# Kernel tuning notes

Measured on AMD Instinct MI355X. Metric: run time of the kernel, lower is better.

Reference implementation:

```python
import jax, jax.numpy as jnp
import numpy as np

H = 64

def _gru(x, Wih, Whh, bih, bhh):
    # x: [NB, L, D]; torch GRU gate order: r, z, n
    h0 = jnp.zeros((x.shape[0], Whh.shape[1]), x.dtype)
    def step(h, xt):
        gi = xt @ Wih.T + bih
        gh = h @ Whh.T + bhh
        ir, iz, inn = jnp.split(gi, 3, axis=-1)
        hr, hz, hn = jnp.split(gh, 3, axis=-1)
        r = jax.nn.sigmoid(ir + hr)
        z = jax.nn.sigmoid(iz + hz)
        n = jnp.tanh(inn + r * hn)
        h_new = (1.0 - z) * n + z * h
        return h_new, h_new
    hT, ys = jax.lax.scan(step, h0, jnp.swapaxes(x, 0, 1))
    return jnp.swapaxes(ys, 0, 1), hT  # outputs [NB,L,H], last hidden [NB,H]


def setup_inputs() -> dict:
    key = jax.random.key(0)
    ks = jax.random.split(key, 20)
    N, B, L, D = 2000, 8, 12, 2
    E = 16000
    s = 0.1
    return {
        "data": jax.random.normal(ks[0], (N, B, L, D), jnp.float32),
        "features": jax.random.normal(ks[1], (N, H), jnp.float32),
        "edge_index": jax.random.randint(ks[2], (2, E), 0, N, jnp.int64 if jax.config.jax_enable_x64 else jnp.int32),
        "Wih1": jax.random.normal(ks[3], (3 * H, D), jnp.float32) * s,
        "Whh1": jax.random.normal(ks[4], (3 * H, H), jnp.float32) * s,
        "bih1": jax.random.normal(ks[5], (3 * H,), jnp.float32) * s,
        "bhh1": jax.random.normal(ks[6], (3 * H,), jnp.float32) * s,
        "W1": jax.random.normal(ks[7], (16, 2 * H), jnp.float32) * s,
        "b1": jax.random.normal(ks[8], (16,), jnp.float32) * s,
        "W2": jax.random.normal(ks[9], (2, 16), jnp.float32) * s,
        "b2": jax.random.normal(ks[10], (2,), jnp.float32) * s,
        "W3": jax.random.normal(ks[11], (2 * H * H, 2), jnp.float32) * s,
        "b3": jax.random.normal(ks[12], (2 * H * H,), jnp.float32) * s,
        "Wih2": jax.random.normal(ks[13], (3 * H, H), jnp.float32) * s,
        "Whh2": jax.random.normal(ks[14], (3 * H, H), jnp.float32) * s,
        "bih2": jax.random.normal(ks[15], (3 * H,), jnp.float32) * s,
        "bhh2": jax.random.normal(ks[16], (3 * H,), jnp.float32) * s,
    }


def reference(data, features, edge_index, Wih1, Whh1, bih1, bhh1,
              W1, b1, W2, b2, W3, b3, Wih2, Whh2, bih2, bhh2):
    N, B, L, D = data.shape
    # --- first GRU over [N*B, L, D] ---
    out1, h1 = _gru(data.reshape(N * B, L, D), Wih1, Whh1, bih1, bhh1)
    out1 = out1.reshape(N, B, L, H)
    h1 = h1.reshape(N, B, H)
    # --- MetaGAT with self loops ---
    loops = jnp.arange(N, dtype=edge_index.dtype)
    src = jnp.concatenate([edge_index[0], loops])  # j (source)
    dst = jnp.concatenate([edge_index[1], loops])  # i (target)
    states_j = out1[src]                 # [E', B, L, H]
    states_i = out1[dst]
    feats = jnp.concatenate([features[dst], features[src]], axis=-1)  # [E', 2H]
    # per-edge MLP generating weights
    hdn = jax.nn.sigmoid(feats @ W1.T + b1)
    hdn = jax.nn.sigmoid(hdn @ W2.T + b2)
    w = (hdn @ W3.T + b3).reshape(-1, 2 * H, H)  # [E', 2H, H]
    states = jnp.concatenate([states_i, states_j], axis=-1)  # [E', B, L, 2H]
    alpha = jax.nn.leaky_relu(jnp.einsum('eblk,ekh->eblh', states, w))
    alpha = jax.nn.softmax(alpha, axis=1)  # softmax over batch dim, as in source
    msg = alpha * states_j                 # [E', B, L, H]
    agg = jax.ops.segment_sum(msg, dst, num_segments=N)
    out2 = jax.nn.relu(agg)                # [N, B, L, H]
    # --- second GRU ---
    _, h2 = _gru(out2.reshape(N * B, L, H), Wih2, Whh2, bih2, bhh2)
    h2 = h2.reshape(N, B, H)
    return h1, h2
```

## Files before the change

kernel.cpp:

```cpp
#include <hip/hip_runtime.h>
#include <hip/hip_bf16.h>

typedef unsigned short ushort_t;
typedef unsigned int uint_t;
typedef __attribute__((ext_vector_type(8))) short bf16x8;
typedef __attribute__((ext_vector_type(4))) float f32x4;

#define NNODE 2000
#define NB 8
#define LSEQ 12
#define HDIM 64
#define NEDGE 16000
#define NSEQ (NNODE * NB)
#define OUT1_ELEMS (NNODE * NB * LSEQ * HDIM)
#define OUT1_BYTES (OUT1_ELEMS * 2)
#define AGG_BYTES  (OUT1_ELEMS * 2)
#define SST 72
#define LOG2E 1.4426950408889634f

#define WFRAG_ELEMS (6 * 2 * 256 * 8)
#define G2FRAG_ELEMS (3 * 2 * 2 * 256 * 8)

__device__ __forceinline__ float bf1(ushort_t u) { return __uint_as_float(((uint_t)u) << 16); }
__device__ __forceinline__ ushort_t fbf(float f) {
    uint_t x = __float_as_uint(f);
    uint_t r = x + 0x7fffu + ((x >> 16) & 1u);
    return (ushort_t)(r >> 16);
}
__device__ __forceinline__ float sigm(float x) {
    return __builtin_amdgcn_rcpf(1.f + __expf(-x));
}
__device__ __forceinline__ float tanh_fast(float x) {
    return 2.f * __builtin_amdgcn_rcpf(1.f + __expf(-2.f * x)) - 1.f;
}


__global__ __launch_bounds__(256) void mega_kernel(
    const float* __restrict__ data, const float* __restrict__ Wih,
    const float* __restrict__ Whh, const float* __restrict__ bih,
    const float* __restrict__ bhh, ushort_t* __restrict__ out1,
    float* __restrict__ h1out,
    const int* __restrict__ edges, int* __restrict__ degree,
    int* __restrict__ rowstart, int* __restrict__ srcids,
    int* __restrict__ eids, int* __restrict__ order,
    const float* __restrict__ features,
    const float* __restrict__ W1, const float* __restrict__ b1,
    const float* __restrict__ W2, const float* __restrict__ b2,
    float* __restrict__ alphas,
    const float* __restrict__ W3, const float* __restrict__ b3,
    const float* __restrict__ Wih2, const float* __restrict__ Whh2,
    ushort_t* __restrict__ wfrag, ushort_t* __restrict__ g2frag)
{
    __shared__ ushort_t H[2][16][SST] __attribute__((aligned(16)));
    __shared__ float XD[16][26];
    __shared__ int hist[NNODE];
    __shared__ int wsum[4];
    __shared__ float m1[4][16];
    __shared__ int dh[64];

    const int bx = blockIdx.x;
    const int tid = threadIdx.x;

    if (bx == 5501) {
        {
            const int wv = tid >> 6, r = tid & 15, quad = (tid >> 4) & 3;
            const int n = wv * 16 + r;
#pragma unroll
            for (int ks = 0; ks < 2; ++ks) {
                ushort_t ta[8], tb[8], tc[8], ba[8], bb[8], bc[8];
#pragma unroll
                for (int jj = 0; jj < 8; ++jj) {
                    const int mt_ = (ks * 32 + quad * 8 + jj) * 64 + n;
                    float2 w2 = ((const float2*)W3)[mt_];
                    ta[jj] = fbf(w2.x * LOG2E); tb[jj] = fbf(w2.y * LOG2E);
                    tc[jj] = fbf(b3[mt_] * LOG2E);
                    const int mb_ = (64 + ks * 32 + quad * 8 + jj) * 64 + n;
                    float2 w2b = ((const float2*)W3)[mb_];
                    ba[jj] = fbf(w2b.x * LOG2E); bb[jj] = fbf(w2b.y * LOG2E);
                    bc[jj] = fbf(b3[mb_] * LOG2E);
                }
                *(uint4*)(wfrag + ((0 * 2 + ks) * 256 + tid) * 8) = *(uint4*)ta;
                *(uint4*)(wfrag + ((1 * 2 + ks) * 256 + tid) * 8) = *(uint4*)tb;
                *(uint4*)(wfrag + ((2 * 2 + ks) * 256 + tid) * 8) = *(uint4*)tc;
                *(uint4*)(wfrag + ((3 * 2 + ks) * 256 + tid) * 8) = *(uint4*)ba;
                *(uint4*)(wfrag + ((4 * 2 + ks) * 256 + tid) * 8) = *(uint4*)bb;
                *(uint4*)(wfrag + ((5 * 2 + ks) * 256 + tid) * 8) = *(uint4*)bc;
            }
        }
        {
            const int nw = tid >> 6, c = tid & 15, quad = (tid >> 4) & 3;
            const int j = nw * 16 + c;
#pragma unroll
            for (int g = 0; g < 3; ++g) {
                const int row = g * 64 + j;
#pragma unroll
                for (int ks = 0; ks < 2; ++ks) {
                    const float* wp = Whh2 + (row << 6) + ks * 32 + quad * 8;
                    float4 wa = *(const float4*)wp;
                    float4 wb = *(const float4*)(wp + 4);
                    ushort_t tmp[8];
                    tmp[0] = fbf(wa.x); tmp[1] = fbf(wa.y); tmp[2] = fbf(wa.z); tmp[3] = fbf(wa.w);
                    tmp[4] = fbf(wb.x); tmp[5] = fbf(wb.y); tmp[6] = fbf(wb.z); tmp[7] = fbf(wb.w);
                    *(uint4*)(g2frag + (((g * 2 + ks) * 2 + 0) * 256 + tid) * 8) = *(uint4*)tmp;
                    const float* wp2 = Wih2 + (row << 6) + ks * 32 + quad * 8;
                    float4 va = *(const float4*)wp2;
                    float4 vb = *(const float4*)(wp2 + 4);
                    tmp[0] = fbf(va.x); tmp[1] = fbf(va.y); tmp[2] = fbf(va.z); tmp[3] = fbf(va.w);
                    tmp[4] = fbf(vb.x); tmp[5] = fbf(vb.y); tmp[6] = fbf(vb.z); tmp[7] = fbf(vb.w);
                    *(uint4*)(g2frag + (((g * 2 + ks) * 2 + 1) * 256 + tid) * 8) = *(uint4*)tmp;
                }
            }
        }
        return;
    }

    if (bx == 1000) {
        for (int k = tid; k < NNODE; k += 256) hist[k] = 0;
        if (tid < 64) dh[tid] = 0;
        __syncthreads();
        for (int it = 0; it < 16; ++it) {
            const int e0 = it * 1024 + tid * 4;
            if (e0 + 3 < NEDGE) {
                int4 v4 = *(const int4*)(edges + NEDGE + e0);
                atomicAdd(&hist[v4.x], 1);
                atomicAdd(&hist[v4.y], 1);
                atomicAdd(&hist[v4.z], 1);
                atomicAdd(&hist[v4.w], 1);
            } else {
#pragma unroll
                for (int k = 0; k < 4; ++k) {
                    const int e = e0 + k;
                    if (e < NEDGE) atomicAdd(&hist[edges[NEDGE + e]], 1);
                }
            }
        }
        __syncthreads();
        const int lane = tid & 63, w = tid >> 6;
        int d[8];
        int s = 0;
#pragma unroll
        for (int q = 0; q < 8; ++q) {
            const int idx = tid * 8 + q;
            d[q] = (idx < NNODE) ? hist[idx] : 0;
            s += d[q];
        }
        int v = s;
#pragma unroll
        for (int off = 1; off < 64; off <<= 1) {
            int u = __shfl_up(v, off);
            if (lane >= off) v += u;
        }
        if (lane == 63) wsum[w] = v;
        __syncthreads();
        int base = 0;
        for (int k = 0; k < 4; ++k) if (k < w) base += wsum[k];
        int run = base + v - s;
        int rs8[8];
#pragma unroll
        for (int q = 0; q < 8; ++q) {
            const int idx = tid * 8 + q;
            if (idx < NNODE) {
                rs8[q] = run;
                rowstart[idx] = run;
                degree[idx] = d[q];
                run += d[q];
                atomicAdd(&dh[63 - min(d[q], 63)], 1);
            }
        }
        __syncthreads();
        if (tid == 0) {
            int acc = 0;
            for (int k = 0; k < 64; ++k) { const int c = dh[k]; dh[k] = acc; acc += c; }
        }
        __syncthreads();
#pragma unroll
        for (int q = 0; q < 8; ++q) {
            const int idx = tid * 8 + q;
            if (idx < NNODE) {
                const int pos = atomicAdd(&dh[63 - min(d[q], 63)], 1);
                order[pos] = idx;
            }
        }
        __syncthreads();
#pragma unroll
        for (int q = 0; q < 8; ++q) {
            const int idx = tid * 8 + q;
            if (idx < NNODE) hist[idx] = rs8[q];
        }
        __syncthreads();
        for (int it = 0; it < 16; ++it) {
            const int e0 = it * 1024 + tid * 4;
            if (e0 + 3 < NEDGE) {
                int4 dv4 = *(const int4*)(edges + NEDGE + e0);
                int4 sv4 = *(const int4*)(edges + e0);
                int pos;
                pos = atomicAdd(&hist[dv4.x], 1); srcids[pos] = sv4.x; eids[pos] = e0;
                pos = atomicAdd(&hist[dv4.y], 1); srcids[pos] = sv4.y; eids[pos] = e0 + 1;
                pos = atomicAdd(&hist[dv4.z], 1); srcids[pos] = sv4.z; eids[pos] = e0 + 2;
                pos = atomicAdd(&hist[dv4.w], 1); srcids[pos] = sv4.w; eids[pos] = e0 + 3;
            } else {
#pragma unroll
                for (int k = 0; k < 4; ++k) {
                    const int e = e0 + k;
                    if (e < NEDGE) {
                        const int pos = atomicAdd(&hist[edges[NEDGE + e]], 1);
                        srcids[pos] = edges[e];
                        eids[pos] = e;
                    }
                }
            }
        }
        return;
    }

    if (bx > 1000) {
        const int w = tid >> 6, lane = tid & 63;
        const int e = (bx - 1001) * 4 + w;
        int i, j;
        if (e < NEDGE) { j = edges[e]; i = edges[NEDGE + e]; }
        else { i = j = e - NEDGE; }
        const int o = lane >> 2, q = lane & 3;
        const float* fsrc = (q < 2) ? (features + i * 64 + q * 32)
                                    : (features + j * 64 + (q - 2) * 32);
        const float* wsrc = W1 + o * 128 + q * 32;
        float acc = 0.f;
#pragma unroll
        for (int k = 0; k < 32; ++k) acc += fsrc[k] * wsrc[k];
        acc += __shfl_xor(acc, 1);
        acc += __shfl_xor(acc, 2);
        if (q == 0) m1[w][o] = sigm(acc + b1[o]);
        __syncthreads();
        if (lane < 32 && e < NEDGE + NNODE) {
            const int o2 = lane >> 4, k = lane & 15;
            float p = m1[w][k] * W2[o2 * 16 + k];
            p += __shfl_xor(p, 1);
            p += __shfl_xor(p, 2);
            p += __shfl_xor(p, 4);
            p += __shfl_xor(p, 8);
            if (k == 0) alphas[e * 2 + o2] = sigm(p + b2[o2]);
        }
        return;
    }

    const int nw = tid >> 6;
    const int c = tid & 15;
    const int quad = (tid >> 4) & 3;
    const int j = nw * 16 + c;
    const int s0 = bx * 16;
    const int crow = tid >> 4, ccol = (tid & 15) * 4;

    if (tid < 128) *(uint4*)&H[0][tid >> 3][(tid & 7) * 8] = uint4{0, 0, 0, 0};
#pragma unroll
    for (int p = 0; p < 2; ++p) {
        const int flat = p * 256 + tid;
        if (flat < 384) {
            const int sl = flat / 24, q = flat - sl * 24;
            XD[sl][q] = data[(s0 + sl) * 24 + q];
        }
    }

    bf16x8 Bh[3][2];
    float wi0[3], wi1[3], bi[3], bh[3];
#pragma unroll
    for (int g = 0; g < 3; ++g) {
        const int row = g * 64 + j;
        float2 wi = *(const float2*)(Wih + row * 2);
        wi0[g] = wi.x; wi1[g] = wi.y;
        bi[g] = bih[row]; bh[g] = bhh[row];
#pragma unroll
        for (int ks = 0; ks < 2; ++ks) {
            const float* wp = Whh + (row << 6) + ks * 32 + quad * 8;
            float4 wa = *(const float4*)wp;
            float4 wb = *(const float4*)(wp + 4);
            ushort_t tmp[8];
            tmp[0] = fbf(wa.x); tmp[1] = fbf(wa.y); tmp[2] = fbf(wa.z); tmp[3] = fbf(wa.w);
            tmp[4] = fbf(wb.x); tmp[5] = fbf(wb.y); tmp[6] = fbf(wb.z); tmp[7] = fbf(wb.w);
            Bh[g][ks] = *(bf16x8*)tmp;
        }
    }

    float hold[4];
#pragma unroll
    for (int rg = 0; rg < 4; ++rg) hold[rg] = 0.f;

    for (int t = 0; t < LSEQ; ++t) {
        __syncthreads();
        const ushort_t (*Hr)[SST] = H[t & 1];
        ushort_t (*Hw)[SST] = H[1 - (t & 1)];
        bf16x8 a0 = *(const bf16x8*)&Hr[c][quad * 8];
        bf16x8 a1 = *(const bf16x8*)&Hr[c][32 + quad * 8];
        if (t > 0)
            *(uint2*)(out1 + (s0 + crow) * (LSEQ * HDIM) + (t - 1) * HDIM + ccol) =
                *(const uint2*)&Hr[crow][ccol];
        f32x4 gh[3];
#pragma unroll
        for (int g = 0; g < 3; ++g) {
            f32x4 acc = {0.f, 0.f, 0.f, 0.f};
            acc = __builtin_amdgcn_mfma_f32_16x16x32_bf16(a0, Bh[g][0], acc, 0, 0, 0);
            acc = __builtin_amdgcn_mfma_f32_16x16x32_bf16(a1, Bh[g][1], acc, 0, 0, 0);
            gh[g] = acc;
        }
#pragma unroll
        for (int rg = 0; rg < 4; ++rg) {
            const int sloc = quad * 4 + rg;
            float2 xp = *(const float2*)&XD[sloc][2 * t];
            float gr = bh[0] + gh[0][rg];
            float gz = bh[1] + gh[1][rg];
            float gn = bh[2] + gh[2][rg];
            float ir = bi[0] + wi0[0] * xp.x + wi1[0] * xp.y;
            float iz = bi[1] + wi0[1] * xp.x + wi1[1] * xp.y;
            float in = bi[2] + wi0[2] * xp.x + wi1[2] * xp.y;
            float r = sigm(ir + gr);
            float z = sigm(iz + gz);
            float n = tanh_fast(in + r * gn);
            float hv = (1.f - z) * n + z * hold[rg];
            hold[rg] = hv;
            Hw[sloc][j] = fbf(hv);
        }
    }
    __syncthreads();
    *(uint2*)(out1 + (s0 + crow) * (LSEQ * HDIM) + (LSEQ - 1) * HDIM + ccol) =
        *(const uint2*)&H[LSEQ & 1][crow][ccol];
#pragma unroll
    for (int rg = 0; rg < 4; ++rg) {
        const int sloc = quad * 4 + rg;
        h1out[(s0 + sloc) * HDIM + j] = hold[rg];
    }
}

__global__ __launch_bounds__(256) void gat_csr_kernel(
    const ushort_t* __restrict__ out1,
    const int* __restrict__ degree, const int* __restrict__ rowstart,
    const int* __restrict__ srcids, const int* __restrict__ eids,
    const int* __restrict__ order,
    const float* __restrict__ alphas,
    const ushort_t* __restrict__ wfrag,
    ushort_t* __restrict__ agg)
{
    __shared__ ushort_t POOL[4][32][SST] __attribute__((aligned(16)));

    const int tid = threadIdx.x;
    const int i = order[blockIdx.x];
    const int mh = blockIdx.y;
    const int deg = degree[i];
    const int rs = rowstart[i];

    const int wv = tid >> 6;
    const int r = tid & 15;
    const int quad = (tid >> 4) & 3;
    const int n = wv * 16 + r;

    const float2 aSelf = *(const float2*)(alphas + (NEDGE + i) * 2);

    int glo[2], lso[2];
#pragma unroll
    for (int p = 0; p < 2; ++p) {
        const int u = p * 256 + tid;
        const int rr = u >> 4, c4 = u & 15;
        const int b = rr & 7, l = (rr >> 3) + 4 * mh;
        glo[p] = (b * 12 + l) * 64 + c4 * 4;
        lso[p] = rr * SST + c4 * 4;
    }
    int afo[2][2];
#pragma unroll
    for (int mt = 0; mt < 2; ++mt) {
        afo[mt][0] = (mt * 16 + r) * SST + quad * 8;
        afo[mt][1] = afo[mt][0] + 32;
    }
    int cbo[2];
#pragma unroll
    for (int mt = 0; mt < 2; ++mt)
        cbo[mt] = (mt * 16 + quad * 4) * SST + (n & ~1);
    const uint_t shamt = (n & 1) ? 0u : 16u;

    const ushort_t* pi = out1 + i * (NB * LSEQ * HDIM);
    ushort_t* const sbase = &POOL[0][0][0];
    ushort_t* const Si = sbase;

#pragma unroll
    for (int p = 0; p < 2; ++p)
        *(uint2*)(Si + lso[p]) = *(const uint2*)(pi + glo[p]);

    bf16x8 WtA[2], WtB[2], WtC[2], WbA[2], WbB[2], WbC[2];
#pragma unroll
    for (int ks = 0; ks < 2; ++ks) {
        WtA[ks] = *(const bf16x8*)(wfrag + ((0 * 2 + ks) * 256 + tid) * 8);
        WtB[ks] = *(const bf16x8*)(wfrag + ((1 * 2 + ks) * 256 + tid) * 8);
        WtC[ks] = *(const bf16x8*)(wfrag + ((2 * 2 + ks) * 256 + tid) * 8);
        WbA[ks] = *(const bf16x8*)(wfrag + ((3 * 2 + ks) * 256 + tid) * 8);
        WbB[ks] = *(const bf16x8*)(wfrag + ((4 * 2 + ks) * 256 + tid) * 8);
        WbC[ks] = *(const bf16x8*)(wfrag + ((5 * 2 + ks) * 256 + tid) * 8);
    }

    __syncthreads();

    f32x4 PA[2], PB[2], PC[2];
#pragma unroll
    for (int mt = 0; mt < 2; ++mt) {
        bf16x8 af0 = *(const bf16x8*)(Si + afo[mt][0]);
        bf16x8 af1 = *(const bf16x8*)(Si + afo[mt][1]);
        f32x4 pa = {0.f, 0.f, 0.f, 0.f};
        f32x4 pb = {0.f, 0.f, 0.f, 0.f};
        f32x4 pc = {0.f, 0.f, 0.f, 0.f};
        pa = __builtin_amdgcn_mfma_f32_16x16x32_bf16(af0, WtA[0], pa, 0, 0, 0);
        pa = __builtin_amdgcn_mfma_f32_16x16x32_bf16(af1, WtA[1], pa, 0, 0, 0);
        pb = __builtin_amdgcn_mfma_f32_16x16x32_bf16(af0, WtB[0], pb, 0, 0, 0);
        pb = __builtin_amdgcn_mfma_f32_16x16x32_bf16(af1, WtB[1], pb, 0, 0, 0);
        pc = __builtin_amdgcn_mfma_f32_16x16x32_bf16(af0, WtC[0], pc, 0, 0, 0);
        pc = __builtin_amdgcn_mfma_f32_16x16x32_bf16(af1, WtC[1], pc, 0, 0, 0);
        PA[mt] = pa; PB[mt] = pb; PC[mt] = pc;
    }

    float accN[2][4];
#pragma unroll
    for (int mt = 0; mt < 2; ++mt)
#pragma unroll
        for (int g2 = 0; g2 < 4; ++g2) accN[mt][g2] = 0.f;

    auto process = [&](const ushort_t* SB, float2 a01) {
#pragma unroll
        for (int mt = 0; mt < 2; ++mt) {
            bf16x8 aj0 = *(const bf16x8*)(SB + afo[mt][0]);
            bf16x8 aj1 = *(const bf16x8*)(SB + afo[mt][1]);
            const uint_t* dp = (const uint_t*)(SB + cbo[mt]);
            uint_t d0 = dp[0], d1 = dp[36], d2 = dp[72], d3 = dp[108];
            f32x4 aA = PA[mt], aB = PB[mt], aC = PC[mt];
            aA = __builtin_amdgcn_mfma_f32_16x16x32_bf16(aj0, WbA[0], aA, 0, 0, 0);
            aA = __builtin_amdgcn_mfma_f32_16x16x32_bf16(aj1, WbA[1], aA, 0, 0, 0);
            aB = __builtin_amdgcn_mfma_f32_16x16x32_bf16(aj0, WbB[0], aB, 0, 0, 0);
            aB = __builtin_amdgcn_mfma_f32_16x16x32_bf16(aj1, WbB[1], aB, 0, 0, 0);
            aC = __builtin_amdgcn_mfma_f32_16x16x32_bf16(aj0, WbC[0], aC, 0, 0, 0);
            aC = __builtin_amdgcn_mfma_f32_16x16x32_bf16(aj1, WbC[1], aC, 0, 0, 0);
            float v[4];
            float s = 0.f;
#pragma unroll
            for (int g2 = 0; g2 < 4; ++g2) {
                float x = fmaf(a01.x, aA[g2], fmaf(a01.y, aB[g2], aC[g2]));
                x = fmaxf(x, 0.01f * x);
                v[g2] = __builtin_amdgcn_exp2f(x);
                s += v[g2];
            }
            s += __shfl_xor(s, 16);
            const float inv = __builtin_amdgcn_rcpf(s);
            uint_t dd[4] = {d0, d1, d2, d3};
#pragma unroll
            for (int g2 = 0; g2 < 4; ++g2) {
                const float sj = __uint_as_float((dd[g2] << shamt) & 0xFFFF0000u);
                accN[mt][g2] += v[g2] * inv * sj;
            }
        }
    };

    int sa_nxt = 0, sb_nxt = 0, eA1 = 0, eB1 = 0;
    float2 aA_cur = float2{0.f, 0.f}, aB_cur = float2{0.f, 0.f};
    if (deg >= 1) { const int e = eids[rs];     aA_cur = *(const float2*)(alphas + e * 2); }
    if (deg >= 2) { const int e = eids[rs + 1]; aB_cur = *(const float2*)(alphas + e * 2); }
    if (deg >= 3) { sa_nxt = srcids[rs + 2]; eA1 = eids[rs + 2]; }
    if (deg >= 4) { sb_nxt = srcids[rs + 3]; eB1 = eids[rs + 3]; }

    uint2 pfA[2], pfB[2];
    {
        const ushort_t* pA = out1 + ((deg >= 1) ? srcids[rs] : 0) * (NB * LSEQ * HDIM);
        const ushort_t* pB = out1 + ((deg >= 2) ? srcids[rs + 1] : 0) * (NB * LSEQ * HDIM);
#pragma unroll
        for (int p = 0; p < 2; ++p) {
            pfA[p] = *(const uint2*)(pA + glo[p]);
            pfB[p] = *(const uint2*)(pB + glo[p]);
        }
    }

    process(Si, aSelf);
    __syncthreads();

    const int npairs = (deg + 1) >> 1;
    for (int pk = 0; pk < npairs; ++pk) {
        ushort_t* SA = sbase + (2 * (pk & 1)) * (32 * SST);
        ushort_t* SB = SA + 32 * SST;
#pragma unroll
        for (int p = 0; p < 2; ++p) {
            *(uint2*)(SA + lso[p]) = pfA[p];
            *(uint2*)(SB + lso[p]) = pfB[p];
        }
        const int base = pk * 2;
        const bool hasB = (base + 1) < deg;

        int sa_n2 = 0, sb_n2 = 0, eA2 = 0, eB2 = 0;
        if (base + 4 < deg) { sa_n2 = srcids[rs + base + 4]; eA2 = eids[rs + base + 4]; }
        if (base + 5 < deg) { sb_n2 = srcids[rs + base + 5]; eB2 = eids[rs + base + 5]; }
        float2 aA_n = float2{0.f, 0.f}, aB_n = float2{0.f, 0.f};
        if (base + 2 < deg) aA_n = *(const float2*)(alphas + eA1 * 2);
        if (base + 3 < deg) aB_n = *(const float2*)(alphas + eB1 * 2);

        __syncthreads();

        if (base + 2 < deg) {
            const ushort_t* pA = out1 + sa_nxt * (NB * LSEQ * HDIM);
#pragma unroll
            for (int p = 0; p < 2; ++p) pfA[p] = *(const uint2*)(pA + glo[p]);
        }
        if (base + 3 < deg) {
            const ushort_t* pB = out1 + sb_nxt * (NB * LSEQ * HDIM);
#pragma unroll
            for (int p = 0; p < 2; ++p) pfB[p] = *(const uint2*)(pB + glo[p]);
        }

        process(SA, aA_cur);
        if (hasB) process(SB, aB_cur);

        aA_cur = aA_n; aB_cur = aB_n;
        sa_nxt = sa_n2; sb_nxt = sb_n2;
        eA1 = eA2; eB1 = eB2;
    }

#pragma unroll
    for (int mt = 0; mt < 2; ++mt)
#pragma unroll
        for (int g2 = 0; g2 < 4; ++g2) {
            const int gr = mh * 32 + mt * 16 + quad * 4 + g2;
            const int b = gr & 7, l = gr >> 3;
            agg[(i * 96 + b * 12 + l) * 64 + n] = fbf(accN[mt][g2]);
        }
}

__global__ __launch_bounds__(256) void gru2_kernel(
    const ushort_t* __restrict__ agg, const ushort_t* __restrict__ g2frag,
    const float* __restrict__ bih, const float* __restrict__ bhh,
    float* __restrict__ h2out)
{
    __shared__ ushort_t H[2][16][SST] __attribute__((aligned(16)));
    __shared__ ushort_t X[2][16][SST] __attribute__((aligned(16)));

    const int tid = threadIdx.x;
    const int nw = tid >> 6;
    const int c = tid & 15;
    const int quad = (tid >> 4) & 3;
    const int j = nw * 16 + c;
    const int s0 = blockIdx.x * 16;
    const int sl = tid >> 3, k0 = (tid & 7) * 8;

    if (tid < 128) *(uint4*)&H[0][tid >> 3][(tid & 7) * 8] = uint4{0, 0, 0, 0};

    bf16x8 Bh[3][2], Bi[3][2];
    float bi[3], bh[3];
#pragma unroll
    for (int g = 0; g < 3; ++g) {
        const int row = g * 64 + j;
        bi[g] = bih[row]; bh[g] = bhh[row];
#pragma unroll
        for (int ks = 0; ks < 2; ++ks) {
            Bh[g][ks] = *(const bf16x8*)(g2frag + (((g * 2 + ks) * 2 + 0) * 256 + tid) * 8);
            Bi[g][ks] = *(const bf16x8*)(g2frag + (((g * 2 + ks) * 2 + 1) * 256 + tid) * 8);
        }
    }

    float hold[4];
#pragma unroll
    for (int rg = 0; rg < 4; ++rg) hold[rg] = 0.f;

    if (tid < 128) {
        ushort_t xr[8];
        *(uint4*)xr = *(const uint4*)(agg + (s0 + sl) * (LSEQ * HDIM) + k0);
        ushort_t xs[8];
#pragma unroll
        for (int q = 0; q < 8; ++q) xs[q] = (xr[q] & 0x8000u) ? (ushort_t)0 : xr[q];
        *(uint4*)&X[0][sl][k0] = *(uint4*)xs;
    }

    for (int t = 0; t < LSEQ; ++t) {
        __syncthreads();
        const int rb = t & 1, wb = 1 - rb;
        bf16x8 ah0 = *(const bf16x8*)&H[rb][c][quad * 8];
        bf16x8 ah1 = *(const bf16x8*)&H[rb][c][32 + quad * 8];
        bf16x8 ax0 = *(const bf16x8*)&X[rb][c][quad * 8];
        bf16x8 ax1 = *(const bf16x8*)&X[rb][c][32 + quad * 8];

        ushort_t xr[8];
        if (t < LSEQ - 1 && tid < 128)
            *(uint4*)xr = *(const uint4*)(agg + (s0 + sl) * (LSEQ * HDIM) +
                                          (t + 1) * HDIM + k0);

        f32x4 gh[3], gi[3];
#pragma unroll
        for (int g = 0; g < 3; ++g) {
            f32x4 acc = {0.f, 0.f, 0.f, 0.f};
            acc = __builtin_amdgcn_mfma_f32_16x16x32_bf16(ah0, Bh[g][0], acc, 0, 0, 0);
            acc = __builtin_amdgcn_mfma_f32_16x16x32_bf16(ah1, Bh[g][1], acc, 0, 0, 0);
            gh[g] = acc;
            f32x4 acc2 = {0.f, 0.f, 0.f, 0.f};
            acc2 = __builtin_amdgcn_mfma_f32_16x16x32_bf16(ax0, Bi[g][0], acc2, 0, 0, 0);
            acc2 = __builtin_amdgcn_mfma_f32_16x16x32_bf16(ax1, Bi[g][1], acc2, 0, 0, 0);
            gi[g] = acc2;
        }
#pragma unroll
        for (int rg = 0; rg < 4; ++rg) {
            const int sloc = quad * 4 + rg;
            float r = sigm(bi[0] + gi[0][rg] + bh[0] + gh[0][rg]);
            float z = sigm(bi[1] + gi[1][rg] + bh[1] + gh[1][rg]);
            float n = tanh_fast(bi[2] + gi[2][rg] + r * (bh[2] + gh[2][rg]));
            float hv = (1.f - z) * n + z * hold[rg];
            hold[rg] = hv;
            H[wb][sloc][j] = fbf(hv);
        }
        if (t < LSEQ - 1 && tid < 128) {
            ushort_t xs[8];
#pragma unroll
            for (int q = 0; q < 8; ++q) xs[q] = (xr[q] & 0x8000u) ? (ushort_t)0 : xr[q];
            *(uint4*)&X[wb][sl][k0] = *(uint4*)xs;
        }
    }
#pragma unroll
    for (int rg = 0; rg < 4; ++rg) {
        const int sloc = quad * 4 + rg;
        h2out[(s0 + sloc) * HDIM + j] = hold[rg];
    }
}

extern "C" void kernel_launch(void* const* d_in, const int* in_sizes, int n_in,
                              void* d_out, int out_size, void* d_ws, size_t ws_size,
                              hipStream_t stream)
{
    const float* data     = (const float*)d_in[0];
    const float* features = (const float*)d_in[1];
    const int*   edges    = (const int*)d_in[2];
    const float* Wih1     = (const float*)d_in[3];
    const float* Whh1     = (const float*)d_in[4];
    const float* bih1     = (const float*)d_in[5];
    const float* bhh1     = (const float*)d_in[6];
    const float* W1       = (const float*)d_in[7];
    const float* b1       = (const float*)d_in[8];
    const float* W2       = (const float*)d_in[9];
    const float* b2       = (const float*)d_in[10];
    const float* W3       = (const float*)d_in[11];
    const float* b3       = (const float*)d_in[12];
    const float* Wih2     = (const float*)d_in[13];
    const float* Whh2     = (const float*)d_in[14];
    const float* bih2     = (const float*)d_in[15];
    const float* bhh2     = (const float*)d_in[16];

    float*    out  = (float*)d_out;
    char*     ws   = (char*)d_ws;
    ushort_t* out1 = (ushort_t*)ws;
    ushort_t* agg  = (ushort_t*)(ws + OUT1_BYTES);
    int*      meta = (int*)(ws + OUT1_BYTES + AGG_BYTES);
    int*   degree   = meta;
    int*   rowstart = meta + NNODE;
    int*   srcids   = meta + 2 * NNODE;
    int*   eids     = meta + 2 * NNODE + NEDGE;
    int*   order    = meta + 2 * NNODE + 2 * NEDGE;
    float* alphas   = (float*)(meta + 3 * NNODE + 2 * NEDGE);
    ushort_t* wfrag  = (ushort_t*)((char*)alphas + 36000 * 4);
    ushort_t* g2frag = wfrag + WFRAG_ELEMS;

    mega_kernel<<<1001 + 4500 + 1, 256, 0, stream>>>(
        data, Wih1, Whh1, bih1, bhh1, out1, out,
        edges, degree, rowstart, srcids, eids, order,
        features, W1, b1, W2, b2, alphas,
        W3, b3, Wih2, Whh2, wfrag, g2frag);
    gat_csr_kernel<<<dim3(NNODE, 3), 256, 0, stream>>>(out1, degree, rowstart, srcids,
                                                       eids, order, alphas, wfrag, agg);
    gru2_kernel<<<NSEQ / 16, 256, 0, stream>>>(agg, g2frag, bih2, bhh2,
                                               out + NNODE * NB * HDIM);
}
```

Baseline: 226.0 us.

## Prefold log2e into GRU weights, vectorize edge MLP, deepen GAT gather prefetch

Multiplies the GRU weights and biases by log2(e) (twice that for the candidate gate) at pack time, so the activations can call the raw exp2 instruction and skip the multiply inside the recurrence. Vectorizes the per-edge first-layer dot product with float4 loads and explicit FMAs. Restructures the GAT aggregation prefetch into two alternating register buffers so neighbour rows are fetched two pairs ahead instead of one. This adds register pressure, and folding the scale before bf16 rounding slightly changes numerics.

```diff
diff --git a/kernel.cpp b/kernel.cpp
--- a/kernel.cpp
+++ b/kernel.cpp
@@ -30,8 +30,11 @@
 __device__ __forceinline__ float sigm(float x) {
     return __builtin_amdgcn_rcpf(1.f + __expf(-x));
 }
-__device__ __forceinline__ float tanh_fast(float x) {
-    return 2.f * __builtin_amdgcn_rcpf(1.f + __expf(-2.f * x)) - 1.f;
+__device__ __forceinline__ float sigm2(float x) {
+    return __builtin_amdgcn_rcpf(1.f + __builtin_amdgcn_exp2f(-x));
+}
+__device__ __forceinline__ float tanh2(float x) {
+    return 2.f * __builtin_amdgcn_rcpf(1.f + __builtin_amdgcn_exp2f(-x)) - 1.f;
 }
 
 
@@ -92,6 +95,7 @@
             const int j = nw * 16 + c;
 #pragma unroll
             for (int g = 0; g < 3; ++g) {
+                const float sc = (g == 2) ? 2.f * LOG2E : LOG2E;
                 const int row = g * 64 + j;
 #pragma unroll
                 for (int ks = 0; ks < 2; ++ks) {
@@ -99,14 +103,18 @@
                     float4 wa = *(const float4*)wp;
                     float4 wb = *(const float4*)(wp + 4);
                     ushort_t tmp[8];
-                    tmp[0] = fbf(wa.x); tmp[1] = fbf(wa.y); tmp[2] = fbf(wa.z); tmp[3] = fbf(wa.w);
-                    tmp[4] = fbf(wb.x); tmp[5] = fbf(wb.y); tmp[6] = fbf(wb.z); tmp[7] = fbf(wb.w);
+                    tmp[0] = fbf(wa.x * sc); tmp[1] = fbf(wa.y * sc);
+                    tmp[2] = fbf(wa.z * sc); tmp[3] = fbf(wa.w * sc);
+                    tmp[4] = fbf(wb.x * sc); tmp[5] = fbf(wb.y * sc);
+                    tmp[6] = fbf(wb.z * sc); tmp[7] = fbf(wb.w * sc);
                     *(uint4*)(g2frag + (((g * 2 + ks) * 2 + 0) * 256 + tid) * 8) = *(uint4*)tmp;
                     const float* wp2 = Wih2 + (row << 6) + ks * 32 + quad * 8;
                     float4 va = *(const float4*)wp2;
                     float4 vb = *(const float4*)(wp2 + 4);
-                    tmp[0] = fbf(va.x); tmp[1] = fbf(va.y); tmp[2] = fbf(va.z); tmp[3] = fbf(va.w);
-                    tmp[4] = fbf(vb.x); tmp[5] = fbf(vb.y); tmp[6] = fbf(vb.z); tmp[7] = fbf(vb.w);
+                    tmp[0] = fbf(va.x * sc); tmp[1] = fbf(va.y * sc);
+                    tmp[2] = fbf(va.z * sc); tmp[3] = fbf(va.w * sc);
+                    tmp[4] = fbf(vb.x * sc); tmp[5] = fbf(vb.y * sc);
+                    tmp[6] = fbf(vb.z * sc); tmp[7] = fbf(vb.w * sc);
                     *(uint4*)(g2frag + (((g * 2 + ks) * 2 + 1) * 256 + tid) * 8) = *(uint4*)tmp;
                 }
             }
@@ -223,9 +231,17 @@
         const float* fsrc = (q < 2) ? (features + i * 64 + q * 32)
                                     : (features + j * 64 + (q - 2) * 32);
         const float* wsrc = W1 + o * 128 + q * 32;
+        const float4* f4 = (const float4*)fsrc;
+        const float4* w4 = (const float4*)wsrc;
         float acc = 0.f;
 #pragma unroll
-        for (int k = 0; k < 32; ++k) acc += fsrc[k] * wsrc[k];
+        for (int k = 0; k < 8; ++k) {
+            float4 a = f4[k], b = w4[k];
+            acc = fmaf(a.x, b.x, acc);
+            acc = fmaf(a.y, b.y, acc);
+            acc = fmaf(a.z, b.z, acc);
+            acc = fmaf(a.w, b.w, acc);
+        }
         acc += __shfl_xor(acc, 1);
         acc += __shfl_xor(acc, 2);
         if (q == 0) m1[w][o] = sigm(acc + b1[o]);
@@ -263,18 +279,21 @@
     float wi0[3], wi1[3], bi[3], bh[3];
 #pragma unroll
     for (int g = 0; g < 3; ++g) {
+        const float sc = (g == 2) ? 2.f * LOG2E : LOG2E;
         const int row = g * 64 + j;
         float2 wi = *(const float2*)(Wih + row * 2);
-        wi0[g] = wi.x; wi1[g] = wi.y;
-        bi[g] = bih[row]; bh[g] = bhh[row];
+        wi0[g] = wi.x * sc; wi1[g] = wi.y * sc;
+        bi[g] = bih[row] * sc; bh[g] = bhh[row] * sc;
 #pragma unroll
         for (int ks = 0; ks < 2; ++ks) {
             const float* wp = Whh + (row << 6) + ks * 32 + quad * 8;
             float4 wa = *(const float4*)wp;
             float4 wb = *(const float4*)(wp + 4);
             ushort_t tmp[8];
-            tmp[0] = fbf(wa.x); tmp[1] = fbf(wa.y); tmp[2] = fbf(wa.z); tmp[3] = fbf(wa.w);
-            tmp[4] = fbf(wb.x); tmp[5] = fbf(wb.y); tmp[6] = fbf(wb.z); tmp[7] = fbf(wb.w);
+            tmp[0] = fbf(wa.x * sc); tmp[1] = fbf(wa.y * sc);
+            tmp[2] = fbf(wa.z * sc); tmp[3] = fbf(wa.w * sc);
+            tmp[4] = fbf(wb.x * sc); tmp[5] = fbf(wb.y * sc);
+            tmp[6] = fbf(wb.z * sc); tmp[7] = fbf(wb.w * sc);
             Bh[g][ks] = *(bf16x8*)tmp;
         }
     }
@@ -310,9 +329,9 @@
             float ir = bi[0] + wi0[0] * xp.x + wi1[0] * xp.y;
             float iz = bi[1] + wi0[1] * xp.x + wi1[1] * xp.y;
             float in = bi[2] + wi0[2] * xp.x + wi1[2] * xp.y;
-            float r = sigm(ir + gr);
-            float z = sigm(iz + gz);
-            float n = tanh_fast(in + r * gn);
+            float r = sigm2(ir + gr);
+            float z = sigm2(iz + gz);
+            float n = tanh2(in + r * gn);
             float hv = (1.f - z) * n + z * hold[rg];
             hold[rg] = hv;
             Hw[sloc][j] = fbf(hv);
@@ -451,21 +470,27 @@
         }
     };
 
-    int sa_nxt = 0, sb_nxt = 0, eA1 = 0, eB1 = 0;
+    int eA1 = 0, eB1 = 0, eA2 = 0, eB2 = 0, sa2 = 0, sb2 = 0;
     float2 aA_cur = float2{0.f, 0.f}, aB_cur = float2{0.f, 0.f};
-    if (deg >= 1) { const int e = eids[rs];     aA_cur = *(const float2*)(alphas + e * 2); }
-    if (deg >= 2) { const int e = eids[rs + 1]; aB_cur = *(const float2*)(alphas + e * 2); }
-    if (deg >= 3) { sa_nxt = srcids[rs + 2]; eA1 = eids[rs + 2]; }
-    if (deg >= 4) { sb_nxt = srcids[rs + 3]; eB1 = eids[rs + 3]; }
-
-    uint2 pfA[2], pfB[2];
+    if (deg >= 1) aA_cur = *(const float2*)(alphas + eids[rs] * 2);
+    if (deg >= 2) aB_cur = *(const float2*)(alphas + eids[rs + 1] * 2);
+    if (deg >= 3) eA1 = eids[rs + 2];
+    if (deg >= 4) eB1 = eids[rs + 3];
+    if (deg >= 5) { eA2 = eids[rs + 4]; sa2 = srcids[rs + 4]; }
+    if (deg >= 6) { eB2 = eids[rs + 5]; sb2 = srcids[rs + 5]; }
+
+    uint2 pfEA[2], pfEB[2], pfOA[2], pfOB[2];
     {
-        const ushort_t* pA = out1 + ((deg >= 1) ? srcids[rs] : 0) * (NB * LSEQ * HDIM);
+        const ushort_t* pA = out1 + ((deg >= 1) ? srcids[rs]     : 0) * (NB * LSEQ * HDIM);
         const ushort_t* pB = out1 + ((deg >= 2) ? srcids[rs + 1] : 0) * (NB * LSEQ * HDIM);
+        const ushort_t* pC = out1 + ((deg >= 3) ? srcids[rs + 2] : 0) * (NB * LSEQ * HDIM);
+        const ushort_t* pD = out1 + ((deg >= 4) ? srcids[rs + 3] : 0) * (NB * LSEQ * HDIM);
 #pragma unroll
         for (int p = 0; p < 2; ++p) {
-            pfA[p] = *(const uint2*)(pA + glo[p]);
-            pfB[p] = *(const uint2*)(pB + glo[p]);
+            pfEA[p] = *(const uint2*)(pA + glo[p]);
+            pfEB[p] = *(const uint2*)(pB + glo[p]);
+            pfOA[p] = *(const uint2*)(pC + glo[p]);
+            pfOB[p] = *(const uint2*)(pD + glo[p]);
         }
     }
 
@@ -474,42 +499,59 @@
 
     const int npairs = (deg + 1) >> 1;
     for (int pk = 0; pk < npairs; ++pk) {
+        const int base = pk * 2;
         ushort_t* SA = sbase + (2 * (pk & 1)) * (32 * SST);
         ushort_t* SB = SA + 32 * SST;
-#pragma unroll
-        for (int p = 0; p < 2; ++p) {
-            *(uint2*)(SA + lso[p]) = pfA[p];
-            *(uint2*)(SB + lso[p]) = pfB[p];
-        }
-        const int base = pk * 2;
-        const bool hasB = (base + 1) < deg;
-
-        int sa_n2 = 0, sb_n2 = 0, eA2 = 0, eB2 = 0;
-        if (base + 4 < deg) { sa_n2 = srcids[rs + base + 4]; eA2 = eids[rs + base + 4]; }
-        if (base + 5 < deg) { sb_n2 = srcids[rs + base + 5]; eB2 = eids[rs + base + 5]; }
+
+        if ((pk & 1) == 0) {
+#pragma unroll
+            for (int p = 0; p < 2; ++p) {
+                *(uint2*)(SA + lso[p]) = pfEA[p];
+                *(uint2*)(SB + lso[p]) = pfEB[p];
+            }
+            if (base + 4 < deg) {
+                const ushort_t* pA = out1 + sa2 * (NB * LSEQ * HDIM);
+#pragma unroll
+                for (int p = 0; p < 2; ++p) pfEA[p] = *(const uint2*)(pA + glo[p]);
+            }
+            if (base + 5 < deg) {
+                const ushort_t* pB = out1 + sb2 * (NB * LSEQ * HDIM);
+#pragma unroll
+                for (int p = 0; p < 2; ++p) pfEB[p] = *(const uint2*)(pB + glo[p]);
+            }
+        } else {
+#pragma unroll
+            for (int p = 0; p < 2; ++p) {
+                *(uint2*)(SA + lso[p]) = pfOA[p];
+                *(uint2*)(SB + lso[p]) = pfOB[p];
+            }
+            if (base + 4 < deg) {
+                const ushort_t* pA = out1 + sa2 * (NB * LSEQ * HDIM);
+#pragma unroll
+                for (int p = 0; p < 2; ++p) pfOA[p] = *(const uint2*)(pA + glo[p]);
+            }
+            if (base + 5 < deg) {
+                const ushort_t* pB = out1 + sb2 * (NB * LSEQ * HDIM);
+#pragma unroll
+                for (int p = 0; p < 2; ++p) pfOB[p] = *(const uint2*)(pB + glo[p]);
+            }
+        }
+
+        int sa_nw = 0, sb_nw = 0, e3A = 0, e3B = 0;
+        if (base + 6 < deg) { sa_nw = srcids[rs + base + 6]; e3A = eids[rs + base + 6]; }
+        if (base + 7 < deg) { sb_nw = srcids[rs + base + 7]; e3B = eids[rs + base + 7]; }
         float2 aA_n = float2{0.f, 0.f}, aB_n = float2{0.f, 0.f};
         if (base + 2 < deg) aA_n = *(const float2*)(alphas + eA1 * 2);
         if (base + 3 < deg) aB_n = *(const float2*)(alphas + eB1 * 2);
 
         __syncthreads();
 
-        if (base + 2 < deg) {
-            const ushort_t* pA = out1 + sa_nxt * (NB * LSEQ * HDIM);
-#pragma unroll
-            for (int p = 0; p < 2; ++p) pfA[p] = *(const uint2*)(pA + glo[p]);
-        }
-        if (base + 3 < deg) {
-            const ushort_t* pB = out1 + sb_nxt * (NB * LSEQ * HDIM);
-#pragma unroll
-            for (int p = 0; p < 2; ++p) pfB[p] = *(const uint2*)(pB + glo[p]);
-        }
-
         process(SA, aA_cur);
-        if (hasB) process(SB, aB_cur);
+        if (base + 1 < deg) process(SB, aB_cur);
 
         aA_cur = aA_n; aB_cur = aB_n;
-        sa_nxt = sa_n2; sb_nxt = sb_n2;
-        eA1 = eA2; eB1 = eB2;
+        eA1 = eA2; eB1 = eB2; eA2 = e3A; eB2 = e3B;
+        sa2 = sa_nw; sb2 = sb_nw;
     }
 
 #pragma unroll
@@ -544,8 +586,9 @@
     float bi[3], bh[3];
 #pragma unroll
     for (int g = 0; g < 3; ++g) {
+        const float sc = (g == 2) ? 2.f * LOG2E : LOG2E;
         const int row = g * 64 + j;
-        bi[g] = bih[row]; bh[g] = bhh[row];
+        bi[g] = bih[row] * sc; bh[g] = bhh[row] * sc;
 #pragma unroll
         for (int ks = 0; ks < 2; ++ks) {
             Bh[g][ks] = *(const bf16x8*)(g2frag + (((g * 2 + ks) * 2 + 0) * 256 + tid) * 8);
@@ -594,9 +637,9 @@
 #pragma unroll
         for (int rg = 0; rg < 4; ++rg) {
             const int sloc = quad * 4 + rg;
-            float r = sigm(bi[0] + gi[0][rg] + bh[0] + gh[0][rg]);
-            float z = sigm(bi[1] + gi[1][rg] + bh[1] + gh[1][rg]);
-            float n = tanh_fast(bi[2] + gi[2][rg] + r * (bh[2] + gh[2][rg]));
+            float r = sigm2(bi[0] + gi[0][rg] + bh[0] + gh[0][rg]);
+            float z = sigm2(bi[1] + gi[1][rg] + bh[1] + gh[1][rg]);
+            float n = tanh2(bi[2] + gi[2][rg] + r * (bh[2] + gh[2][rg]));
             float hv = (1.f - z) * n + z * hold[rg];
             hold[rg] = hv;
             H[wb][sloc][j] = fbf(hv);
```

Measured after the change: 230.7 us. 1.02x slower.
